# Performance work log

Measured on AMD Instinct MI355X. Metric: run time of the kernel, lower is better.

Reference implementation:

```python
import jax, jax.numpy as jnp
import numpy as np
import math

D_MODEL = 1024
NUM_HEADS = 16
HEAD_DIM = D_MODEL // NUM_HEADS  # 64
THETA = 10000.0
BATCH = 2
SEQ = 2048


def setup_inputs() -> dict:
    key = jax.random.key(0)
    ks = jax.random.split(key, 5)
    scale = 0.02
    return {
        "in_features": jax.random.normal(ks[0], (BATCH, SEQ, D_MODEL), jnp.float32),
        "q_proj": jax.random.normal(ks[1], (D_MODEL, D_MODEL), jnp.float32) * scale,
        "k_proj": jax.random.normal(ks[2], (D_MODEL, D_MODEL), jnp.float32) * scale,
        "v_proj": jax.random.normal(ks[3], (D_MODEL, D_MODEL), jnp.float32) * scale,
        "o_proj": jax.random.normal(ks[4], (D_MODEL, D_MODEL), jnp.float32) * scale,
        "token_positions": jnp.arange(SEQ, dtype=jnp.int32),
    }


def _rope(x, token_positions):
    # x: [b, h, s, head_dim]; interleaved even/odd rotation
    half = HEAD_DIM // 2
    inv_freq = 1.0 / (THETA ** (2.0 * jnp.arange(half, dtype=x.dtype) / HEAD_DIM))
    angle = token_positions.astype(x.dtype)[:, None] * inv_freq[None, :]  # [s, half]
    cos, sin = jnp.cos(angle), jnp.sin(angle)
    x_e, x_o = x[..., ::2], x[..., 1::2]
    r_e = x_e * cos - x_o * sin
    r_o = x_e * sin + x_o * cos
    # interleave back: [..., s, half, 2] -> [..., s, head_dim]
    return jnp.stack([r_e, r_o], axis=-1).reshape(x.shape)


def reference(in_features, q_proj, k_proj, v_proj, o_proj, token_positions):
    b, s, _ = in_features.shape
    # projections: weight layout is [d_out, d_in]
    Q = jnp.einsum('bsd,kd->bsk', in_features, q_proj)
    K = jnp.einsum('bsd,kd->bsk', in_features, k_proj)
    V = jnp.einsum('bsd,kd->bsk', in_features, v_proj)
    # split heads: [b, h, s, head_dim]
    Q = Q.reshape(b, s, NUM_HEADS, HEAD_DIM).transpose(0, 2, 1, 3)
    K = K.reshape(b, s, NUM_HEADS, HEAD_DIM).transpose(0, 2, 1, 3)
    V = V.reshape(b, s, NUM_HEADS, HEAD_DIM).transpose(0, 2, 1, 3)
    Q = _rope(Q, token_positions)
    K = _rope(K, token_positions)
    scores = jnp.einsum('bhnd,bhmd->bhnm', Q, K) / math.sqrt(HEAD_DIM)
    causal = jnp.tril(jnp.ones((s, s), dtype=bool))  # [s, s]
    scores = jnp.where(causal[None, None], scores, -jnp.inf)
    attn = jax.nn.softmax(scores, axis=-1)
    out = jnp.einsum('bhnm,bhmd->bhnd', attn, V)
    out = out.transpose(0, 2, 1, 3).reshape(b, s, D_MODEL)
    return jnp.einsum('bsv,dv->bsd', out, o_proj)
```

## Files before the change

kernel.cpp:

```cpp
#include <hip/hip_runtime.h>
#include <hip/hip_bf16.h>

#define D_MODEL 1024
#define NHEAD   16
#define HDIM    64
#define SEQQ    2048
#define NBATCH  2
#define MROWS   (NBATCH * SEQQ)

typedef unsigned short u16;
typedef __attribute__((ext_vector_type(8))) short short8;
typedef __attribute__((ext_vector_type(4))) float floatx4;

__device__ __forceinline__ u16 f2b(float f) {
    union { __hip_bfloat16 h; u16 u; } cv;
    cv.h = __float2bfloat16(f);
    return cv.u;
}
__device__ __forceinline__ float b2f(u16 u) {
    return __uint_as_float(((unsigned int)u) << 16);
}
__device__ __forceinline__ short8 load8(const u16* p) {
    return *reinterpret_cast<const short8*>(p);
}
__device__ __forceinline__ void async_cp16(const void* g, void* l) {
    __builtin_amdgcn_global_load_lds(
        (const __attribute__((address_space(1))) void*)g,
        (__attribute__((address_space(3))) void*)l, 16, 0, 0);
}

__global__ void cvt_all(const float* __restrict__ X,
                        const float* __restrict__ w0, const float* __restrict__ w1,
                        const float* __restrict__ w2, const float* __restrict__ w3,
                        u16* __restrict__ xo,
                        u16* __restrict__ o0, u16* __restrict__ o1,
                        u16* __restrict__ o2, u16* __restrict__ o3) {
    const int z = blockIdx.y;
    const int n4 = (D_MODEL * D_MODEL) / 4;
    const float* in;
    u16* out;
    if (z < 4) { in = X + (size_t)z * n4 * 4;  out = xo + (size_t)z * n4 * 4; }
    else {
        in  = (z == 4) ? w0 : (z == 5) ? w1 : (z == 6) ? w2 : w3;
        out = (z == 4) ? o0 : (z == 5) ? o1 : (z == 6) ? o2 : o3;
    }
    const int i = blockIdx.x * 256 + threadIdx.x;
    float4 v = reinterpret_cast<const float4*>(in)[i];
    ushort4 o;
    o.x = f2b(v.x); o.y = f2b(v.y); o.z = f2b(v.z); o.w = f2b(v.w);
    reinterpret_cast<ushort4*>(out)[i] = o;
}

template <int WRITE_F32>
__global__ __launch_bounds__(256) void gemm_bt(
    const u16* __restrict__ A,
    const u16* __restrict__ B0, const u16* __restrict__ B1, const u16* __restrict__ B2,
    void* __restrict__ C0, void* __restrict__ C1, void* __restrict__ C2,
    int M, int N, int K)
{
    const u16* Bt = (blockIdx.z == 0) ? B0 : (blockIdx.z == 1 ? B1 : B2);
    void*      Cp = (blockIdx.z == 0) ? C0 : (blockIdx.z == 1 ? C1 : C2);

    __shared__ __attribute__((aligned(16))) u16 As[128 * 32];
    __shared__ __attribute__((aligned(16))) u16 Bs[128 * 32];

    const int tid  = threadIdx.x;
    const int w    = tid >> 6;
    const int lane = tid & 63;
    const int l15  = lane & 15;
    const int quad = lane >> 4;
    const int wm   = w >> 1, wn = w & 1;
    const int tm   = blockIdx.x * 128, tn = blockIdx.y * 128;

    floatx4 acc[4][4];
#pragma unroll
    for (int i = 0; i < 4; i++)
#pragma unroll
        for (int j = 0; j < 4; j++) {
            floatx4 z = {0.f, 0.f, 0.f, 0.f};
            acc[i][j] = z;
        }

    const int srow = lane >> 2;
    const int scol = (lane & 3) * 8;

    for (int k0 = 0; k0 < K; k0 += 32) {
#pragma unroll
        for (int ch = w; ch < 8; ch += 4) {
            async_cp16(A  + (size_t)(tm + ch * 16 + srow) * K + k0 + scol, &As[ch * 512]);
            async_cp16(Bt + (size_t)(tn + ch * 16 + srow) * K + k0 + scol, &Bs[ch * 512]);
        }
        __syncthreads();

        short8 af[4], bfr[4];
#pragma unroll
        for (int mi = 0; mi < 4; mi++)
            af[mi] = load8(&As[(wm * 64 + mi * 16 + l15) * 32 + quad * 8]);
#pragma unroll
        for (int ni = 0; ni < 4; ni++)
            bfr[ni] = load8(&Bs[(wn * 64 + ni * 16 + l15) * 32 + quad * 8]);
#pragma unroll
        for (int mi = 0; mi < 4; mi++)
#pragma unroll
            for (int ni = 0; ni < 4; ni++)
                acc[mi][ni] = __builtin_amdgcn_mfma_f32_16x16x32_bf16(af[mi], bfr[ni], acc[mi][ni], 0, 0, 0);
        __syncthreads();
    }

#pragma unroll
    for (int mi = 0; mi < 4; mi++)
#pragma unroll
        for (int ni = 0; ni < 4; ni++)
#pragma unroll
            for (int rg = 0; rg < 4; rg++) {
                int row = tm + wm * 64 + mi * 16 + quad * 4 + rg;
                int col = tn + wn * 64 + ni * 16 + l15;
                float v = acc[mi][ni][rg];
                if (WRITE_F32) reinterpret_cast<float*>(Cp)[(size_t)row * N + col] = v;
                else           reinterpret_cast<u16*>(Cp)[(size_t)row * N + col]   = f2b(v);
            }
}

__global__ void rope_qk(const u16* __restrict__ Qraw, const u16* __restrict__ Kraw,
                        const int* __restrict__ pos, u16* __restrict__ Qt, u16* __restrict__ Kt)
{
    const int gid = blockIdx.x * 256 + threadIdx.x;
    const int j = gid & 31;
    const int s = (gid >> 5) & (SEQQ - 1);
    const int h = (gid >> 16) & (NHEAD - 1);
    const int b = gid >> 20;

    const float p   = (float)pos[s];
    const float inv = expf(-(float)j * (9.210340371976184f / 32.0f));
    float sn, cs;
    sincosf(p * inv, &sn, &cs);

    const size_t ioff = ((size_t)(b * SEQQ + s)) * D_MODEL + h * HDIM + 2 * j;
    const ushort2 qp = *reinterpret_cast<const ushort2*>(&Qraw[ioff]);
    const ushort2 kp = *reinterpret_cast<const ushort2*>(&Kraw[ioff]);
    const float qe = b2f(qp.x), qo = b2f(qp.y);
    const float ke = b2f(kp.x), ko = b2f(kp.y);

    const size_t ooff = (((size_t)(b * NHEAD + h)) * SEQQ + s) * HDIM + 2 * j;
    ushort2 qr;
    qr.x = f2b((qe * cs - qo * sn) * 0.125f);
    qr.y = f2b((qe * sn + qo * cs) * 0.125f);
    ushort2 kr;
    kr.x = f2b(ke * cs - ko * sn);
    kr.y = f2b(ke * sn + ko * cs);
    *reinterpret_cast<ushort2*>(&Qt[ooff]) = qr;
    *reinterpret_cast<ushort2*>(&Kt[ooff]) = kr;
}

__global__ __launch_bounds__(256) void vtrans(const u16* __restrict__ Vraw, u16* __restrict__ Vt)
{
    __shared__ u16 tile[64][65];
    const int s0 = blockIdx.x * 64, h = blockIdx.y, b = blockIdx.z;
    const int t = threadIdx.x;
#pragma unroll
    for (int i = 0; i < 16; i++) {
        int idx = t + i * 256;
        int sl = idx >> 6, dl = idx & 63;
        tile[sl][dl] = Vraw[((size_t)(b * SEQQ + s0 + sl)) * D_MODEL + h * HDIM + dl];
    }
    __syncthreads();
#pragma unroll
    for (int i = 0; i < 16; i++) {
        int idx = t + i * 256;
        int dl = idx >> 6, sl = idx & 63;
        Vt[(((size_t)(b * NHEAD + h)) * HDIM + dl) * SEQQ + s0 + sl] = tile[sl][dl];
    }
}

#define PSTRIDE 72
__global__ __launch_bounds__(512, 6) void attn_kernel(
    const u16* __restrict__ Qt, const u16* __restrict__ Kt, const u16* __restrict__ Vt,
    u16* __restrict__ Out)
{
    const int qblk = (gridDim.x - 1) - blockIdx.x;
    const int h = blockIdx.y, b = blockIdx.z;
    const int tid = threadIdx.x, w = tid >> 6, lane = tid & 63;
    const int l15 = lane & 15, quad = lane >> 4;
    const size_t bh = (size_t)(b * NHEAD + h);
    const u16* Qh = Qt + bh * SEQQ * HDIM;
    const u16* Kh = Kt + bh * SEQQ * HDIM;
    const u16* Vh = Vt + bh * HDIM * SEQQ;
    const int q0w = qblk * 128 + w * 16;
    const int tdiag = q0w >> 6;
    const int tmax  = qblk * 2 + 1;

    __shared__ __attribute__((aligned(16))) u16 Ks[2][64 * 64];
    __shared__ __attribute__((aligned(16))) u16 Vs[2][64 * 64];
    __shared__ __attribute__((aligned(16))) u16 Plds[8][16 * PSTRIDE];

    short8 qf[2];
#pragma unroll
    for (int kk = 0; kk < 2; kk++)
        qf[kk] = load8(&Qh[(size_t)(q0w + l15) * HDIM + kk * 32 + quad * 8]);

    short8 ones;
#pragma unroll
    for (int i = 0; i < 8; i++) ones[i] = (short)0x3F80;

    floatx4 O[4];
    floatx4 l_acc = {0.f, 0.f, 0.f, 0.f};
#pragma unroll
    for (int c = 0; c < 4; c++) { floatx4 z = {0.f, 0.f, 0.f, 0.f}; O[c] = z; }

    const int rr  = lane >> 3;
    const int swz = ((lane & 7) ^ rr) * 8;
    auto stage = [&](int buf, int tt) {
        const int k0s = tt * 64;
        async_cp16(Kh + (size_t)(k0s + w * 8 + rr) * HDIM + swz, &Ks[buf][w * 512]);
        async_cp16(Vh + (size_t)(w * 8 + rr) * SEQQ + k0s + swz, &Vs[buf][w * 512]);
    };

    const int sw1 = ((quad)     ^ (l15 & 7)) * 8;
    const int sw2 = ((quad + 4) ^ (l15 & 7)) * 8;

    stage(0, 0);

    for (int t = 0; t <= tmax; ++t) {
        const int cur = t & 1;
        __syncthreads();
        if (t < tmax) stage(cur ^ 1, t + 1);

        if (t > tdiag) continue;

        const u16* KsB = &Ks[cur][0];
        const u16* VsB = &Vs[cur][0];
        const int k0 = t * 64;

        floatx4 S[4];
#pragma unroll
        for (int c = 0; c < 4; c++) {
            const int rowb = (c * 16 + l15) * 64;
            floatx4 z = {0.f, 0.f, 0.f, 0.f};
            S[c] = __builtin_amdgcn_mfma_f32_16x16x32_bf16(qf[0], load8(&KsB[rowb + sw1]), z,    0, 0, 0);
            S[c] = __builtin_amdgcn_mfma_f32_16x16x32_bf16(qf[1], load8(&KsB[rowb + sw2]), S[c], 0, 0, 0);
        }

        if (t == tdiag) {
#pragma unroll
            for (int r = 0; r < 4; r++) {
                const int q = q0w + quad * 4 + r;
#pragma unroll
                for (int c = 0; c < 4; c++)
                    if (k0 + c * 16 + l15 > q) S[c][r] = -1e30f;
            }
        }

#pragma unroll
        for (int c = 0; c < 4; c++)
#pragma unroll
            for (int r = 0; r < 4; r++)
                S[c][r] = __expf(S[c][r]);

#pragma unroll
        for (int c = 0; c < 4; c++)
#pragma unroll
            for (int r = 0; r < 4; r++)
                Plds[w][(quad * 4 + r) * PSTRIDE + c * 16 + l15] = f2b(S[c][r]);
        const short8 pf0 = load8(&Plds[w][l15 * PSTRIDE + quad * 8]);
        const short8 pf1 = load8(&Plds[w][l15 * PSTRIDE + 32 + quad * 8]);

        l_acc = __builtin_amdgcn_mfma_f32_16x16x32_bf16(pf0, ones, l_acc, 0, 0, 0);
        l_acc = __builtin_amdgcn_mfma_f32_16x16x32_bf16(pf1, ones, l_acc, 0, 0, 0);

#pragma unroll
        for (int c2 = 0; c2 < 4; c2++) {
            const int rowb = (c2 * 16 + l15) * 64;
            O[c2] = __builtin_amdgcn_mfma_f32_16x16x32_bf16(pf0, load8(&VsB[rowb + sw1]), O[c2], 0, 0, 0);
            O[c2] = __builtin_amdgcn_mfma_f32_16x16x32_bf16(pf1, load8(&VsB[rowb + sw2]), O[c2], 0, 0, 0);
        }
    }

    float inv_l[4];
#pragma unroll
    for (int r = 0; r < 4; r++) inv_l[r] = 1.0f / l_acc[r];

#pragma unroll
    for (int c2 = 0; c2 < 4; c2++)
#pragma unroll
        for (int r = 0; r < 4; r++) {
            const int q   = q0w + quad * 4 + r;
            const int col = h * HDIM + c2 * 16 + l15;
            Out[(size_t)(b * SEQQ + q) * D_MODEL + col] = f2b(O[c2][r] * inv_l[r]);
        }
}

extern "C" void kernel_launch(void* const* d_in, const int* in_sizes, int n_in,
                              void* d_out, int out_size, void* d_ws, size_t ws_size,
                              hipStream_t stream)
{
    const float* X  = (const float*)d_in[0];
    const float* Wq = (const float*)d_in[1];
    const float* Wk = (const float*)d_in[2];
    const float* Wv = (const float*)d_in[3];
    const float* Wo = (const float*)d_in[4];
    const int* tpos = (const int*)d_in[5];
    float* out = (float*)d_out;
    char* ws = (char*)d_ws;

    const size_t MB = (size_t)1 << 20;
    u16* Xb   = (u16*)(ws + 0);
    u16* WqB  = (u16*)(ws + 8 * MB);
    u16* WkB  = (u16*)(ws + 10 * MB);
    u16* WvB  = (u16*)(ws + 12 * MB);
    u16* WoB  = (u16*)(ws + 14 * MB);
    u16* Qraw = (u16*)(ws + 16 * MB);
    u16* Kraw = (u16*)(ws + 24 * MB);
    u16* Vraw = (u16*)(ws + 32 * MB);
    u16* Qt   = (u16*)(ws + 40 * MB);
    u16* Kt   = (u16*)(ws + 48 * MB);
    u16* Vt   = Xb;
    u16* AOut = Qraw;

    cvt_all<<<dim3(1024, 8), 256, 0, stream>>>(X, Wq, Wk, Wv, Wo,
                                               Xb, WqB, WkB, WvB, WoB);

    gemm_bt<0><<<dim3(32, 8, 3), 256, 0, stream>>>(Xb, WqB, WkB, WvB,
                                                   Qraw, Kraw, Vraw,
                                                   MROWS, D_MODEL, D_MODEL);
    rope_qk<<<8192, 256, 0, stream>>>(Qraw, Kraw, tpos, Qt, Kt);
    vtrans<<<dim3(32, 16, 2), 256, 0, stream>>>(Vraw, Vt);
    attn_kernel<<<dim3(16, 16, 2), 512, 0, stream>>>(Qt, Kt, Vt, AOut);
    gemm_bt<1><<<dim3(32, 8, 1), 256, 0, stream>>>(AOut, WoB, WoB, WoB,
                                                   out, out, out,
                                                   MROWS, D_MODEL, D_MODEL);
}
```

Measured before the change: 207.2 us.

## Fuse RoPE into QKV GEMM epilogue and retile output projection

Removes the separate rope_qk kernel. RoPE is now applied in the QKV GEMM epilogue, using a cos/sin table built in an extra grid slice of the conversion kernel and lane shuffles to pair even/odd columns. Q and K are written directly in head-major layout. The output projection gets its own kernel with 64-row tiles, doubling the block count for better CU occupancy. The trade-off is scattered 2-byte epilogue stores and per-element table loads in the GEMM.

```diff
diff --git a/kernel.cpp b/kernel.cpp
--- a/kernel.cpp
+++ b/kernel.cpp
@@ -32,10 +32,23 @@
 __global__ void cvt_all(const float* __restrict__ X,
                         const float* __restrict__ w0, const float* __restrict__ w1,
                         const float* __restrict__ w2, const float* __restrict__ w3,
+                        const int* __restrict__ tpos,
                         u16* __restrict__ xo,
                         u16* __restrict__ o0, u16* __restrict__ o1,
-                        u16* __restrict__ o2, u16* __restrict__ o3) {
+                        u16* __restrict__ o2, u16* __restrict__ o3,
+                        float2* __restrict__ tbl) {
     const int z = blockIdx.y;
+    if (z == 8) {
+        const int i = blockIdx.x * 256 + threadIdx.x;
+        if (i >= SEQQ * 32) return;
+        const int s = i >> 5, j = i & 31;
+        const float p = (float)tpos[s];
+        const float inv = expf(-(float)j * (9.210340371976184f / 32.0f));
+        float sn, cs;
+        sincosf(p * inv, &sn, &cs);
+        tbl[i] = make_float2(cs, sn);
+        return;
+    }
     const int n4 = (D_MODEL * D_MODEL) / 4;
     const float* in;
     u16* out;
@@ -51,15 +64,14 @@
     reinterpret_cast<ushort4*>(out)[i] = o;
 }
 
-template <int WRITE_F32>
-__global__ __launch_bounds__(256) void gemm_bt(
+__global__ __launch_bounds__(256) void gemm_qkv(
     const u16* __restrict__ A,
     const u16* __restrict__ B0, const u16* __restrict__ B1, const u16* __restrict__ B2,
-    void* __restrict__ C0, void* __restrict__ C1, void* __restrict__ C2,
-    int M, int N, int K)
-{
+    u16* __restrict__ Qt, u16* __restrict__ Kt, u16* __restrict__ Vraw,
+    const float2* __restrict__ tbl)
+{
+    const int K = D_MODEL, N = D_MODEL;
     const u16* Bt = (blockIdx.z == 0) ? B0 : (blockIdx.z == 1 ? B1 : B2);
-    void*      Cp = (blockIdx.z == 0) ? C0 : (blockIdx.z == 1 ? C1 : C2);
 
     __shared__ __attribute__((aligned(16))) u16 As[128 * 32];
     __shared__ __attribute__((aligned(16))) u16 Bs[128 * 32];
@@ -107,49 +119,44 @@
         __syncthreads();
     }
 
+    if (blockIdx.z == 2) {
+#pragma unroll
+        for (int mi = 0; mi < 4; mi++)
+#pragma unroll
+            for (int ni = 0; ni < 4; ni++)
+#pragma unroll
+                for (int rg = 0; rg < 4; rg++) {
+                    int row = tm + wm * 64 + mi * 16 + quad * 4 + rg;
+                    int col = tn + wn * 64 + ni * 16 + l15;
+                    Vraw[(size_t)row * N + col] = f2b(acc[mi][ni][rg]);
+                }
+        return;
+    }
+
+    const float qscale = (blockIdx.z == 0) ? 0.125f : 1.0f;
+    u16* dst = (blockIdx.z == 0) ? Qt : Kt;
+    const int parity = l15 & 1;
 #pragma unroll
     for (int mi = 0; mi < 4; mi++)
 #pragma unroll
-        for (int ni = 0; ni < 4; ni++)
-#pragma unroll
-            for (int rg = 0; rg < 4; rg++) {
-                int row = tm + wm * 64 + mi * 16 + quad * 4 + rg;
-                int col = tn + wn * 64 + ni * 16 + l15;
-                float v = acc[mi][ni][rg];
-                if (WRITE_F32) reinterpret_cast<float*>(Cp)[(size_t)row * N + col] = v;
-                else           reinterpret_cast<u16*>(Cp)[(size_t)row * N + col]   = f2b(v);
+        for (int rg = 0; rg < 4; rg++) {
+            const int row = tm + wm * 64 + mi * 16 + quad * 4 + rg;
+            const int s  = row & (SEQQ - 1);
+            const int bb = row >> 11;
+#pragma unroll
+            for (int ni = 0; ni < 4; ni++) {
+                const int col  = tn + wn * 64 + ni * 16 + l15;
+                const int dcol = col & 63;
+                const int hh   = col >> 6;
+                const int j    = dcol >> 1;
+                const float2 cssn = tbl[s * 32 + j];
+                const float mine   = acc[mi][ni][rg];
+                const float theirs = __shfl_xor(mine, 1, 64);
+                const float res = parity ? (theirs * cssn.y + mine * cssn.x)
+                                         : (mine * cssn.x - theirs * cssn.y);
+                dst[(((size_t)(bb * NHEAD + hh)) * SEQQ + s) * HDIM + dcol] = f2b(res * qscale);
             }
-}
-
-__global__ void rope_qk(const u16* __restrict__ Qraw, const u16* __restrict__ Kraw,
-                        const int* __restrict__ pos, u16* __restrict__ Qt, u16* __restrict__ Kt)
-{
-    const int gid = blockIdx.x * 256 + threadIdx.x;
-    const int j = gid & 31;
-    const int s = (gid >> 5) & (SEQQ - 1);
-    const int h = (gid >> 16) & (NHEAD - 1);
-    const int b = gid >> 20;
-
-    const float p   = (float)pos[s];
-    const float inv = expf(-(float)j * (9.210340371976184f / 32.0f));
-    float sn, cs;
-    sincosf(p * inv, &sn, &cs);
-
-    const size_t ioff = ((size_t)(b * SEQQ + s)) * D_MODEL + h * HDIM + 2 * j;
-    const ushort2 qp = *reinterpret_cast<const ushort2*>(&Qraw[ioff]);
-    const ushort2 kp = *reinterpret_cast<const ushort2*>(&Kraw[ioff]);
-    const float qe = b2f(qp.x), qo = b2f(qp.y);
-    const float ke = b2f(kp.x), ko = b2f(kp.y);
-
-    const size_t ooff = (((size_t)(b * NHEAD + h)) * SEQQ + s) * HDIM + 2 * j;
-    ushort2 qr;
-    qr.x = f2b((qe * cs - qo * sn) * 0.125f);
-    qr.y = f2b((qe * sn + qo * cs) * 0.125f);
-    ushort2 kr;
-    kr.x = f2b(ke * cs - ko * sn);
-    kr.y = f2b(ke * sn + ko * cs);
-    *reinterpret_cast<ushort2*>(&Qt[ooff]) = qr;
-    *reinterpret_cast<ushort2*>(&Kt[ooff]) = kr;
+        }
 }
 
 __global__ __launch_bounds__(256) void vtrans(const u16* __restrict__ Vraw, u16* __restrict__ Vt)
@@ -289,6 +296,68 @@
         }
 }
 
+__global__ __launch_bounds__(256) void gemm_o(
+    const u16* __restrict__ A, const u16* __restrict__ Bt, float* __restrict__ C)
+{
+    const int K = D_MODEL, N = D_MODEL;
+    __shared__ __attribute__((aligned(16))) u16 As[64 * 32];
+    __shared__ __attribute__((aligned(16))) u16 Bs[128 * 32];
+
+    const int tid  = threadIdx.x;
+    const int w    = tid >> 6;
+    const int lane = tid & 63;
+    const int l15  = lane & 15;
+    const int quad = lane >> 4;
+    const int wm   = w >> 1, wn = w & 1;
+    const int tm   = blockIdx.x * 64, tn = blockIdx.y * 128;
+
+    floatx4 acc[2][4];
+#pragma unroll
+    for (int i = 0; i < 2; i++)
+#pragma unroll
+        for (int j = 0; j < 4; j++) {
+            floatx4 z = {0.f, 0.f, 0.f, 0.f};
+            acc[i][j] = z;
+        }
+
+    const int srow = lane >> 2;
+    const int scol = (lane & 3) * 8;
+
+    for (int k0 = 0; k0 < K; k0 += 32) {
+#pragma unroll
+        for (int ch = w; ch < 12; ch += 4) {
+            if (ch < 4) async_cp16(A  + (size_t)(tm + ch * 16 + srow) * K + k0 + scol, &As[ch * 512]);
+            else        async_cp16(Bt + (size_t)(tn + (ch - 4) * 16 + srow) * K + k0 + scol, &Bs[(ch - 4) * 512]);
+        }
+        __syncthreads();
+
+        short8 af[2], bfr[4];
+#pragma unroll
+        for (int mi = 0; mi < 2; mi++)
+            af[mi] = load8(&As[(wm * 32 + mi * 16 + l15) * 32 + quad * 8]);
+#pragma unroll
+        for (int ni = 0; ni < 4; ni++)
+            bfr[ni] = load8(&Bs[(wn * 64 + ni * 16 + l15) * 32 + quad * 8]);
+#pragma unroll
+        for (int mi = 0; mi < 2; mi++)
+#pragma unroll
+            for (int ni = 0; ni < 4; ni++)
+                acc[mi][ni] = __builtin_amdgcn_mfma_f32_16x16x32_bf16(af[mi], bfr[ni], acc[mi][ni], 0, 0, 0);
+        __syncthreads();
+    }
+
+#pragma unroll
+    for (int mi = 0; mi < 2; mi++)
+#pragma unroll
+        for (int ni = 0; ni < 4; ni++)
+#pragma unroll
+            for (int rg = 0; rg < 4; rg++) {
+                int row = tm + wm * 32 + mi * 16 + quad * 4 + rg;
+                int col = tn + wn * 64 + ni * 16 + l15;
+                C[(size_t)row * N + col] = acc[mi][ni][rg];
+            }
+}
+
 extern "C" void kernel_launch(void* const* d_in, const int* in_sizes, int n_in,
                               void* d_out, int out_size, void* d_ws, size_t ws_size,
                               hipStream_t stream)
@@ -303,29 +372,24 @@
     char* ws = (char*)d_ws;
 
     const size_t MB = (size_t)1 << 20;
-    u16* Xb   = (u16*)(ws + 0);
-    u16* WqB  = (u16*)(ws + 8 * MB);
-    u16* WkB  = (u16*)(ws + 10 * MB);
-    u16* WvB  = (u16*)(ws + 12 * MB);
-    u16* WoB  = (u16*)(ws + 14 * MB);
-    u16* Qraw = (u16*)(ws + 16 * MB);
-    u16* Kraw = (u16*)(ws + 24 * MB);
-    u16* Vraw = (u16*)(ws + 32 * MB);
-    u16* Qt   = (u16*)(ws + 40 * MB);
-    u16* Kt   = (u16*)(ws + 48 * MB);
-    u16* Vt   = Xb;
-    u16* AOut = Qraw;
-
-    cvt_all<<<dim3(1024, 8), 256, 0, stream>>>(X, Wq, Wk, Wv, Wo,
-                                               Xb, WqB, WkB, WvB, WoB);
-
-    gemm_bt<0><<<dim3(32, 8, 3), 256, 0, stream>>>(Xb, WqB, WkB, WvB,
-                                                   Qraw, Kraw, Vraw,
-                                                   MROWS, D_MODEL, D_MODEL);
-    rope_qk<<<8192, 256, 0, stream>>>(Qraw, Kraw, tpos, Qt, Kt);
+    u16*   Xb   = (u16*)(ws + 0);
+    u16*   WqB  = (u16*)(ws + 8 * MB);
+    u16*   WkB  = (u16*)(ws + 10 * MB);
+    u16*   WvB  = (u16*)(ws + 12 * MB);
+    u16*   WoB  = (u16*)(ws + 14 * MB);
+    u16*   AOut = (u16*)(ws + 16 * MB);
+    float2* tbl = (float2*)(ws + 24 * MB);
+    u16*   Vraw = (u16*)(ws + 32 * MB);
+    u16*   Qt   = (u16*)(ws + 40 * MB);
+    u16*   Kt   = (u16*)(ws + 48 * MB);
+    u16*   Vt   = Xb;
+
+    cvt_all<<<dim3(1024, 9), 256, 0, stream>>>(X, Wq, Wk, Wv, Wo, tpos,
+                                               Xb, WqB, WkB, WvB, WoB, tbl);
+
+    gemm_qkv<<<dim3(32, 8, 3), 256, 0, stream>>>(Xb, WqB, WkB, WvB,
+                                                 Qt, Kt, Vraw, tbl);
     vtrans<<<dim3(32, 16, 2), 256, 0, stream>>>(Vraw, Vt);
     attn_kernel<<<dim3(16, 16, 2), 512, 0, stream>>>(Qt, Kt, Vt, AOut);
-    gemm_bt<1><<<dim3(32, 8, 1), 256, 0, stream>>>(AOut, WoB, WoB, WoB,
-                                                   out, out, out,
-                                                   MROWS, D_MODEL, D_MODEL);
-}
+    gemm_o<<<dim3(64, 8), 256, 0, stream>>>(AOut, WoB, out);
+}
```

Measured after the change: 212.9 us. 2.8% more time.
